# Optimization experiments

Measured on AMD Instinct MI355X. Metric: run time of the kernel, lower is better.

The kernel has to match this reference:

```python
import jax, jax.numpy as jnp
import numpy as np

N_SL, H, W, D = 64, 128, 128, 128
D_MODEL, D_INNER, N_LAYERS, N_HEAD = 256, 512, 4, 4
RES_RATIO = 1.0
N_ITER_CG = 2

def _gauss_psf(shape=(3, 3, 3), sigma=1.0):
    ax = [np.arange(s) - (s - 1) / 2.0 for s in shape]
    gz, gy, gx = np.meshgrid(*ax, indexing='ij')
    k = np.exp(-(gx ** 2 + gy ** 2 + gz ** 2) / (2 * sigma ** 2))
    return jnp.asarray((k / k.sum()).astype(np.float32))

def _rigid_transforms():
    rng = np.random.default_rng(0)
    a = rng.uniform(-0.3, 0.3, (N_SL, 3)).astype(np.float32)
    t = rng.uniform(-8.0, 8.0, (N_SL, 3)).astype(np.float32)
    z = np.zeros(N_SL, np.float32); o = np.ones(N_SL, np.float32)
    cz, sz = np.cos(a[:, 2]), np.sin(a[:, 2])
    cy, sy = np.cos(a[:, 1]), np.sin(a[:, 1])
    cx, sx = np.cos(a[:, 0]), np.sin(a[:, 0])
    Rz = np.stack([cz, -sz, z, sz, cz, z, z, z, o], -1).reshape(-1, 3, 3)
    Ry = np.stack([cy, z, sy, z, o, z, -sy, z, cy], -1).reshape(-1, 3, 3)
    Rx = np.stack([o, z, z, z, cx, -sx, z, sx, cx], -1).reshape(-1, 3, 3)
    R = Rz @ Ry @ Rx
    return jnp.asarray(np.concatenate([R, t[:, :, None]], -1).astype(np.float32))

def _slice_points():
    xs = (jnp.arange(W, dtype=jnp.float32) - (W - 1) / 2.0) * RES_RATIO
    ys = (jnp.arange(H, dtype=jnp.float32) - (H - 1) / 2.0) * RES_RATIO
    gy, gx = jnp.meshgrid(ys, xs, indexing='ij')
    return jnp.stack([gx.ravel(), gy.ravel(), jnp.zeros(H * W, jnp.float32)], -1)

def _psf_grid(psf):
    kz, ky, kx = psf.shape
    oz = jnp.arange(kz, dtype=jnp.float32) - (kz - 1) / 2.0
    oy = jnp.arange(ky, dtype=jnp.float32) - (ky - 1) / 2.0
    ox = jnp.arange(kx, dtype=jnp.float32) - (kx - 1) / 2.0
    gz, gy, gx = jnp.meshgrid(oz, oy, ox, indexing='ij')
    return jnp.stack([gx.ravel(), gy.ravel(), gz.ravel()], -1), psf.ravel()

def _tri_gather(vol, c):
    Dz, Dy, Dx = vol.shape
    x, y, z = c[..., 0], c[..., 1], c[..., 2]
    x0, y0, z0 = jnp.floor(x), jnp.floor(y), jnp.floor(z)
    fx, fy, fz = x - x0, y - y0, z - z0
    out = jnp.zeros(x.shape, vol.dtype)
    for dz in (0, 1):
        for dy in (0, 1):
            for dx in (0, 1):
                xi, yi, zi = x0 + dx, y0 + dy, z0 + dz
                w = (fx if dx else 1 - fx) * (fy if dy else 1 - fy) * (fz if dz else 1 - fz)
                ok = (xi >= 0) & (xi < Dx) & (yi >= 0) & (yi < Dy) & (zi >= 0) & (zi < Dz)
                xi = jnp.clip(xi, 0, Dx - 1).astype(jnp.int32)
                yi = jnp.clip(yi, 0, Dy - 1).astype(jnp.int32)
                zi = jnp.clip(zi, 0, Dz - 1).astype(jnp.int32)
                out = out + jnp.where(ok, w * vol[zi, yi, xi], 0.0)
    return out

def _tri_scatter(vflat, c, vals, shape):
    Dz, Dy, Dx = shape
    x, y, z = c[..., 0], c[..., 1], c[..., 2]
    x0, y0, z0 = jnp.floor(x), jnp.floor(y), jnp.floor(z)
    fx, fy, fz = x - x0, y - y0, z - z0
    for dz in (0, 1):
        for dy in (0, 1):
            for dx in (0, 1):
                xi, yi, zi = x0 + dx, y0 + dy, z0 + dz
                w = (fx if dx else 1 - fx) * (fy if dy else 1 - fy) * (fz if dz else 1 - fz)
                ok = (xi >= 0) & (xi < Dx) & (yi >= 0) & (yi < Dy) & (zi >= 0) & (zi < Dz)
                xi = jnp.clip(xi, 0, Dx - 1).astype(jnp.int32)
                yi = jnp.clip(yi, 0, Dy - 1).astype(jnp.int32)
                zi = jnp.clip(zi, 0, Dz - 1).astype(jnp.int32)
                idx = (zi * Dy + yi) * Dx + xi
                vflat = vflat.at[idx.ravel()].add(jnp.where(ok, w * vals, 0.0).ravel())
    return vflat

def _slice_acq(transforms, volume, slices_mask, psf):
    vol = volume[0, 0]
    R, t = transforms[:, :, :3], transforms[:, :, 3]
    pts = _slice_points()
    offs, pw = _psf_grid(psf)
    ctr = jnp.array([(vol.shape[2] - 1) / 2.0, (vol.shape[1] - 1) / 2.0, (vol.shape[0] - 1) / 2.0], jnp.float32)
    def body(acc, ow):
        o, w = ow
        world = jnp.einsum('nij,pj->npi', R, pts + o) + t[:, None, :]
        return acc + w * _tri_gather(vol, world + ctr), None
    acc, _ = jax.lax.scan(jax.checkpoint(body), jnp.zeros((transforms.shape[0], H * W), jnp.float32), (offs, pw))
    out = acc.reshape(-1, 1, H, W)
    if slices_mask is not None:
        out = out * slices_mask
    return out

def _slice_acq_adj(transforms, psf, slices, slices_mask, vol_shape):
    vals = slices.reshape(slices.shape[0], -1)
    if slices_mask is not None:
        vals = vals * slices_mask.reshape(slices.shape[0], -1)
    R, t = transforms[:, :, :3], transforms[:, :, 3]
    pts = _slice_points()
    offs, pw = _psf_grid(psf)
    Dz, Dy, Dx = vol_shape
    ctr = jnp.array([(Dx - 1) / 2.0, (Dy - 1) / 2.0, (Dz - 1) / 2.0], jnp.float32)
    def body(vf, ow):
        o, w = ow
        world = jnp.einsum('nij,pj->npi', R, pts + o) + t[:, None, :] + ctr
        return _tri_scatter(vf, world, w * vals, vol_shape), None
    vf, _ = jax.lax.scan(jax.checkpoint(body), jnp.zeros(Dz * Dy * Dx, jnp.float32), (offs, pw))
    return vf.reshape(1, 1, Dz, Dy, Dx)

def _gaussian_blur(x, sigma=1.0, ks=3):
    ax = np.arange(ks) - (ks - 1) / 2.0
    k1 = np.exp(-ax ** 2 / (2 * sigma ** 2))
    k2 = np.outer(k1, k1); k2 = k2 / k2.sum()
    w = jnp.asarray(k2.astype(np.float32)).reshape(1, 1, ks, ks)
    return jax.lax.conv_general_dilated(x, w, (1, 1), 'SAME', dimension_numbers=('NCHW', 'OIHW', 'NCHW'))

def _conv(x, w, stride=1):
    return jax.lax.conv_general_dilated(x, w, (stride, stride), 'SAME', dimension_numbers=('NCHW', 'OIHW', 'NCHW'))

def _cg(AtA, b, x, n_iter):
    r = b - AtA(x)
    p = r
    rr = jnp.vdot(r, r)
    for _ in range(n_iter):
        Ap = AtA(p)
        alpha = rr / jnp.vdot(p, Ap)
        x = x + alpha * p
        r = r - alpha * Ap
        rr2 = jnp.vdot(r, r)
        p = r + (rr2 / rr) * p
        rr = rr2
    return x

def _ln(x, g, b):
    m = x.mean(-1, keepdims=True)
    v = ((x - m) ** 2).mean(-1, keepdims=True)
    return (x - m) / jnp.sqrt(v + 1e-5) * g + b

def _mha(h, wq, wk, wv, wo):
    n, dm = h.shape
    dk = dm // N_HEAD
    q = (h @ wq).reshape(n, N_HEAD, dk)
    k = (h @ wk).reshape(n, N_HEAD, dk)
    v = (h @ wv).reshape(n, N_HEAD, dk)
    att = jax.nn.softmax(jnp.einsum('qhd,khd->hqk', q, k) / jnp.sqrt(jnp.float32(dk)), -1)
    return jnp.einsum('hqk,khd->qhd', att, v).reshape(n, dm) @ wo

def _forward(theta, transforms, slices, volume, psf, idx, conv1_w, b1_w1, b1_w2, b2_w1, b2_w2, b2_proj, b3_w1, b3_w2, b3_proj, pos_w, pos_b, wq, wk, wv, wo, ln1_g, ln1_b, ff1_w, ff1_b, ff2_w, ff2_b, ln2_g, ln2_b, fc_w, fc_b):
    mask = (_gaussian_blur(slices) > 0).astype(slices.dtype)
    slices_est = _slice_acq(transforms, volume, mask, psf)
    z = jnp.concatenate([slices, slices_est], 1)
    hc = jax.nn.relu(_conv(z, conv1_w, 2))
    r = _conv(jax.nn.relu(_conv(hc, b1_w1)), b1_w2)
    hc = jax.nn.relu(hc + r)
    r = _conv(jax.nn.relu(_conv(hc, b2_w1, 2)), b2_w2)
    hc = jax.nn.relu(_conv(hc, b2_proj, 2) + r)
    r = _conv(jax.nn.relu(_conv(hc, b3_w1, 2)), b3_w2)
    hc = jax.nn.relu(_conv(hc, b3_proj, 2) + r)
    feat = hc.mean((2, 3))
    pe = jnp.concatenate([theta, idx], -1) @ pos_w + pos_b
    hs = feat + pe
    for l in range(N_LAYERS):
        hs = _ln(hs + _mha(hs, wq[l], wk[l], wv[l], wo[l]), ln1_g[l], ln1_b[l])
        ff = jax.nn.relu(hs @ ff1_w[l] + ff1_b[l]) @ ff2_w[l] + ff2_b[l]
        hs = _ln(hs + ff, ln2_g[l], ln2_b[l])
    x = hs @ fc_w + fc_b
    x = jax.nn.softmax(x, axis=0) * x.shape[0]
    x = jnp.minimum(x, 3.0)
    p = x.reshape(-1, 1, 1, 1)
    vol_shape = volume.shape[2:]
    At = lambda s: _slice_acq_adj(transforms, psf, s, mask, vol_shape)
    AtA = lambda v: At(_slice_acq(transforms, v, mask, psf) * p)
    b = At(slices * p)
    vol = _cg(AtA, b, volume, N_ITER_CG)
    return jax.nn.relu(vol), x

def setup_inputs():
    key = jax.random.key(0)
    ks = jax.random.split(key, 24)
    def nrm(k, shp, s=0.05):
        return jax.random.normal(k, shp, jnp.float32) * s
    yy, xx = jnp.meshgrid(jnp.arange(H, dtype=jnp.float32), jnp.arange(W, dtype=jnp.float32), indexing='ij')
    disk = (((yy - (H - 1) / 2) ** 2 + (xx - (W - 1) / 2) ** 2) < (0.45 * W) ** 2).astype(jnp.float32)
    slices = jax.random.uniform(ks[0], (N_SL, 1, H, W), jnp.float32) * disk
    return {
        'theta': nrm(ks[1], (N_SL, 6), 0.1),
        'transforms': _rigid_transforms(),
        'slices': slices,
        'volume': jax.random.uniform(ks[2], (1, 1, D, H, W), jnp.float32) * 0.1,
        'psf': _gauss_psf(),
        'idx': jnp.tile(jnp.arange(N_SL, dtype=jnp.float32).reshape(-1, 1) / N_SL, (1, 2)),
        'conv1_w': nrm(ks[3], (64, 2, 7, 7)),
        'b1_w1': nrm(ks[4], (64, 64, 3, 3)),
        'b1_w2': nrm(ks[5], (64, 64, 3, 3)),
        'b2_w1': nrm(ks[6], (128, 64, 3, 3)),
        'b2_w2': nrm(ks[7], (128, 128, 3, 3)),
        'b2_proj': nrm(ks[8], (128, 64, 1, 1)),
        'b3_w1': nrm(ks[9], (256, 128, 3, 3)),
        'b3_w2': nrm(ks[10], (256, 256, 3, 3)),
        'b3_proj': nrm(ks[11], (256, 128, 1, 1)),
        'pos_w': nrm(ks[12], (8, D_MODEL)),
        'pos_b': jnp.zeros((D_MODEL,), jnp.float32),
        'wq': nrm(ks[13], (N_LAYERS, D_MODEL, D_MODEL)),
        'wk': nrm(ks[14], (N_LAYERS, D_MODEL, D_MODEL)),
        'wv': nrm(ks[15], (N_LAYERS, D_MODEL, D_MODEL)),
        'wo': nrm(ks[16], (N_LAYERS, D_MODEL, D_MODEL)),
        'ln1_g': jnp.ones((N_LAYERS, D_MODEL), jnp.float32),
        'ln1_b': jnp.zeros((N_LAYERS, D_MODEL), jnp.float32),
        'ff1_w': nrm(ks[17], (N_LAYERS, D_MODEL, D_INNER)),
        'ff1_b': jnp.zeros((N_LAYERS, D_INNER), jnp.float32),
        'ff2_w': nrm(ks[18], (N_LAYERS, D_INNER, D_MODEL)),
        'ff2_b': jnp.zeros((N_LAYERS, D_MODEL), jnp.float32),
        'ln2_g': jnp.ones((N_LAYERS, D_MODEL), jnp.float32),
        'ln2_b': jnp.zeros((N_LAYERS, D_MODEL), jnp.float32),
        'fc_w': nrm(ks[19], (D_MODEL, 1)),
        'fc_b': jnp.zeros((1,), jnp.float32),
    }

def reference(theta, transforms, slices, volume, psf, idx, conv1_w, b1_w1, b1_w2, b2_w1, b2_w2, b2_proj, b3_w1, b3_w2, b3_proj, pos_w, pos_b, wq, wk, wv, wo, ln1_g, ln1_b, ff1_w, ff1_b, ff2_w, ff2_b, ln2_g, ln2_b, fc_w, fc_b):
    return _forward(theta, transforms, slices, volume, psf, idx, conv1_w, b1_w1, b1_w2, b2_w1, b2_w2, b2_proj, b3_w1, b3_w2, b3_proj, pos_w, pos_b, wq, wk, wv, wo, ln1_g, ln1_b, ff1_w, ff1_b, ff2_w, ff2_b, ln2_g, ln2_b, fc_w, fc_b)
```

## Files before the change

### kernel.cpp

```cpp
#include <hip/hip_runtime.h>
#include <hip/hip_bf16.h>

#define NSL 64
#define NPX 16384
#define VN  2097152
#define PCL 16900
#define PCS 50700
#define PCN 3244800

__global__ void k_prep(const float* __restrict__ tr, const float* __restrict__ psf,
                       float* __restrict__ Rm, float* __restrict__ pw)
{
  int n = threadIdx.x;
  if (n < 27) pw[n] = psf[n];
  if (n >= NSL) return;
  #pragma unroll
  for (int i = 0; i < 3; i++){
    #pragma unroll
    for (int j = 0; j < 3; j++) Rm[n*12 + i*3 + j] = tr[n*12 + i*4 + j];
    Rm[n*12 + 9 + i] = tr[n*12 + i*4 + 3];
  }
}

__global__ void k_mask(const float* __restrict__ slices, float* __restrict__ mask)
{
  int gid = blockIdx.x*256 + threadIdx.x;
  if (gid >= NSL*NPX) return;
  int n = gid >> 14, p = gid & 16383;
  int py = p >> 7, px = p & 127;
  const float* s = slices + n*NPX;
  bool any = false;
  for (int dy = -1; dy <= 1; dy++){
    int yy = py + dy;
    if ((unsigned)yy >= 128u) continue;
    for (int dx = -1; dx <= 1; dx++){
      int xx = px + dx;
      if ((unsigned)xx >= 128u) continue;
      any = any || (s[yy*128 + xx] > 0.f);
    }
  }
  mask[gid] = any ? 1.f : 0.f;
}

__global__ void k_volcopy(const float* __restrict__ v, float* __restrict__ o)
{
  int gid = blockIdx.x*256 + threadIdx.x;
  if (gid < VN) o[gid] = v[gid];
}

__global__ void k_copy0(const float* __restrict__ slices, float* __restrict__ z)
{
  int gid = blockIdx.x*256 + threadIdx.x;
  if (gid >= NSL*NPX) return;
  int n = gid >> 14, p = gid & 16383;
  z[n*2*NPX + p] = slices[gid];
}

__global__ void k_premul(const float* __restrict__ s, const float* __restrict__ mask,
                         const float* __restrict__ ps, float* __restrict__ o)
{
  int gid = blockIdx.x*256 + threadIdx.x;
  if (gid >= NSL*NPX) return;
  float v = s[gid] * mask[gid];
  if (ps) v *= ps[gid >> 14];
  o[gid] = v;
}

__device__ __forceinline__ float lerpf(float a, float b, float t){ return fmaf(t, b-a, a); }

__device__ __forceinline__ float tri_gather(const float* __restrict__ vol, float x, float y, float z)
{
  float xf = floorf(x), yf = floorf(y), zf = floorf(z);
  int x0 = (int)xf, y0 = (int)yf, z0 = (int)zf;
  float fx = x - xf, fy = y - yf, fz = z - zf;
  if ((unsigned)x0 < 127u && (unsigned)y0 < 127u && (unsigned)z0 < 127u){
    const float* p = vol + (z0*128 + y0)*128 + x0;
    float c00 = lerpf(p[0],     p[1],     fx);
    float c01 = lerpf(p[128],   p[129],   fx);
    float c10 = lerpf(p[16384], p[16385], fx);
    float c11 = lerpf(p[16512], p[16513], fx);
    return lerpf(lerpf(c00, c01, fy), lerpf(c10, c11, fy), fz);
  }
  float gx0 = 1.f - fx, gy0 = 1.f - fy, gz0 = 1.f - fz;
  bool vx0 = (unsigned)x0 < 128u, vx1 = (unsigned)(x0+1) < 128u;
  bool vy0 = (unsigned)y0 < 128u, vy1 = (unsigned)(y0+1) < 128u;
  bool vz0 = (unsigned)z0 < 128u, vz1 = (unsigned)(z0+1) < 128u;
  int i0 = (z0*128 + y0)*128 + x0;
  float acc = 0.f;
  if (vz0){
    if (vy0){
      if (vx0) acc += gx0*gy0*gz0 * vol[i0];
      if (vx1) acc += fx *gy0*gz0 * vol[i0+1];
    }
    if (vy1){
      if (vx0) acc += gx0*fy*gz0 * vol[i0+128];
      if (vx1) acc += fx *fy*gz0 * vol[i0+129];
    }
  }
  if (vz1){
    int i1 = i0 + 16384;
    if (vy0){
      if (vx0) acc += gx0*gy0*fz * vol[i1];
      if (vx1) acc += fx *gy0*fz * vol[i1+1];
    }
    if (vy1){
      if (vx0) acc += gx0*fy*fz * vol[i1+128];
      if (vx1) acc += fx *fy*fz * vol[i1+129];
    }
  }
  return acc;
}

__global__ void k_gather(const float* __restrict__ vol, const float* __restrict__ Rm,
                         const float* __restrict__ pw, const float* __restrict__ mask,
                         const float* __restrict__ ps, float* __restrict__ out,
                         int outStride, int outOff)
{
  int gid = blockIdx.x*256 + threadIdx.x;
  int n = gid >> 14;
  __shared__ float srm[12];
  __shared__ float sdof[27][3];
  __shared__ float spw[27];
  if (threadIdx.x < 12) srm[threadIdx.x] = Rm[n*12 + threadIdx.x];
  __syncthreads();
  if (threadIdx.x < 27){
    int k = threadIdx.x;
    float ox = (float)(k % 3) - 1.f;
    float oy = (float)((k/3) % 3) - 1.f;
    float oz = (float)(k/9) - 1.f;
    sdof[k][0] = srm[0]*ox + srm[1]*oy + srm[2]*oz;
    sdof[k][1] = srm[3]*ox + srm[4]*oy + srm[5]*oz;
    sdof[k][2] = srm[6]*ox + srm[7]*oy + srm[8]*oz;
    spw[k] = pw[k];
  }
  __syncthreads();
  int p = gid & 16383;
  int py = p >> 7, px = p & 127;
  float gx = (float)px - 63.5f, gy = (float)py - 63.5f;
  float bx = srm[0]*gx + srm[1]*gy + srm[9]  + 63.5f;
  float by = srm[3]*gx + srm[4]*gy + srm[10] + 63.5f;
  float bz = srm[6]*gx + srm[7]*gy + srm[11] + 63.5f;
  float acc = 0.f;
  for (int k = 0; k < 27; k += 3){
    float g0 = tri_gather(vol, bx+sdof[k  ][0], by+sdof[k  ][1], bz+sdof[k  ][2]);
    float g1 = tri_gather(vol, bx+sdof[k+1][0], by+sdof[k+1][1], bz+sdof[k+1][2]);
    float g2 = tri_gather(vol, bx+sdof[k+2][0], by+sdof[k+2][1], bz+sdof[k+2][2]);
    acc += spw[k]*g0 + spw[k+1]*g1 + spw[k+2]*g2;
  }
  float v = acc * mask[gid];
  if (ps) v *= ps[n];
  out[n*outStride + outOff + p] = v;
}

__global__ void k_pcorr(const float* __restrict__ val, const float* __restrict__ pw,
                        float* __restrict__ out)
{
  int gid = blockIdx.x*256 + threadIdx.x;
  if (gid >= PCN) return;
  int n = gid / PCS;
  int r = gid % PCS;
  int l = r / PCL;
  int q = r % PCL;
  int my = q / 130 - 1, mx = q % 130 - 1;
  const float* vs = val + n*NPX;
  const float* pg = pw + l*9;
  float inner = 0.f;
  #pragma unroll
  for (int oy = -1; oy <= 1; oy++){
    int qy = my - oy;
    if ((unsigned)qy >= 128u) continue;
    const float* vrow = vs + qy*128;
    const float* pr = pg + (oy+1)*3;
    #pragma unroll
    for (int ox = -1; ox <= 1; ox++){
      int qx = mx - ox;
      if ((unsigned)qx >= 128u) continue;
      inner += pr[ox+1] * vrow[qx];
    }
  }
  out[gid] = inner;
}

__global__ __launch_bounds__(256, 4) void k_sadj(
    const float* __restrict__ pcor,
    const float* __restrict__ Rm,
    float* __restrict__ out)
{
  __shared__ float sR[NSL*12];
  __shared__ int   slist[NSL];
  __shared__ int   scnt;
  int tid = threadIdx.x;
  for (int i = tid; i < NSL*12; i += 256) sR[i] = Rm[i];
  __syncthreads();

  int b  = blockIdx.x;
  int bx = (b & 15) * 8;
  int by = ((b >> 4) & 15) * 8;
  int bz = (b >> 8) * 4;

  if (tid < 64){
    const float* R = &sR[tid*12];
    float axc = ((float)bx + 3.5f) - 63.5f - R[9];
    float ayc = ((float)by + 3.5f) - 63.5f - R[10];
    float azc = ((float)bz + 1.5f) - 63.5f - R[11];
    float Zc = R[2]*axc + R[5]*ayc + R[8]*azc;
    float rZ = fabsf(R[2])*3.5f + fabsf(R[5])*3.5f + fabsf(R[8])*1.5f;
    bool ok = fabsf(Zc) < 2.7321f + rZ;
    if (ok){
      float Pc = R[0]*axc + R[3]*ayc + R[6]*azc + 63.5f;
      float rP = fabsf(R[0])*3.5f + fabsf(R[3])*3.5f + fabsf(R[6])*1.5f;
      float Qc = R[1]*axc + R[4]*ayc + R[7]*azc + 63.5f;
      float rQ = fabsf(R[1])*3.5f + fabsf(R[4])*3.5f + fabsf(R[7])*1.5f;
      ok = (Pc + rP > -2.7321f) && (Pc - rP < 130.7321f)
        && (Qc + rQ > -2.7321f) && (Qc - rQ < 130.7321f);
    }
    unsigned long long m = __ballot(ok);
    if (ok) slist[__popcll(m & ((1ull << tid) - 1ull))] = tid;
    if (tid == 0) scnt = (int)__popcll(m);
  }
  __syncthreads();
  int cnt = scnt;

  int lx = tid & 7, ly = (tid >> 3) & 7, lz = tid >> 6;
  int vx = bx + lx, vy = by + ly, vz = bz + lz;

  float cvx = (float)vx - 63.5f;
  float cvy = (float)vy - 63.5f;
  float cvz = (float)vz - 63.5f;

  float acc = 0.f;
  for (int i = 0; i < cnt; i++){
    int n = slist[i];
    const float* R = &sR[n*12];
    float ax = cvx - R[9], ay = cvy - R[10], az = cvz - R[11];
    float Z = R[2]*ax + R[5]*ay + R[8]*az;
    if (fabsf(Z) >= 2.7321f) continue;
    float P = R[0]*ax + R[3]*ay + R[6]*az + 63.5f;
    float Q = R[1]*ax + R[4]*ay + R[7]*az + 63.5f;
    if (P <= -2.7321f || P >= 130.7321f || Q <= -2.7321f || Q >= 130.7321f) continue;
    const float* pc = pcor + n*PCS;

    #pragma unroll
    for (int mz = -1; mz <= 1; mz++){
      float dz = (float)mz - Z;
      float rem2 = 3.f - dz*dz;
      if (rem2 <= 0.f) continue;
      float sy = sqrtf(rem2);
      int my0 = (int)ceilf(Q - sy), my1 = (int)floorf(Q + sy);
      if (my0 < -1) my0 = -1;
      if (my1 > 128) my1 = 128;
      const float* pl = pc + (mz+1)*PCL;
      for (int my = my0; my <= my1; my++){
        float dy = (float)my - Q;
        float rem1 = rem2 - dy*dy;
        if (rem1 <= 0.f) continue;
        float sx = sqrtf(rem1);
        int mx0 = (int)ceilf(P - sx), mx1 = (int)floorf(P + sx);
        if (mx0 < -1) mx0 = -1;
        if (mx1 > 128) mx1 = 128;
        float dx = (float)mx0 - P;
        float rx = R[0]*dx + R[1]*dy + R[2]*dz;
        float ry = R[3]*dx + R[4]*dy + R[5]*dz;
        float rz = R[6]*dx + R[7]*dy + R[8]*dz;
        const float* crow = pl + (my+1)*130 + (mx0+1);
        for (int mx = mx0; mx <= mx1; mx++){
          float w3 = fmaxf(1.f - fabsf(rx), 0.f)
                   * fmaxf(1.f - fabsf(ry), 0.f)
                   * fmaxf(1.f - fabsf(rz), 0.f);
          if (w3 > 0.f) acc += w3 * crow[mx - mx0];
          rx += R[0]; ry += R[3]; rz += R[6];
        }
      }
    }
  }
  out[(vz*128 + vy)*128 + vx] = acc;
}

template<int K, int S, int TILE, int CC, int COT>
__global__ __launch_bounds__(256, 2) void k_convt(
    const float* __restrict__ in, const float* __restrict__ wt,
    const float* __restrict__ res, float* __restrict__ out,
    int Cin, int Hin, int Cout, int Hout,
    int pad, int relu, int nBG, int spTiles)
{
  constexpr int BPB  = 1024 / (TILE*TILE);
  constexpr int ITX  = (K==1) ? TILE : (TILE-1)*S + K;
  constexpr int ITP  = ITX | 1;
  constexpr int KK   = K*K;
  constexpr int PERB = TILE*TILE/4;
  constexpr int RS   = (K==1) ? 1 : S;
  constexpr int NIN  = (CC*ITX*ITX + PERB - 1)/PERB;
  constexpr int NWT  = (COT*CC*KK + 255)/256;

  __shared__ float sIn[BPB*CC*ITX*ITP];
  __shared__ float sW[CC*KK*COT];

  int tid = threadIdx.x;
  int bl  = tid / PERB;
  int t2  = tid % PERB;
  int tx  = t2 % TILE;
  int tyq = (t2 / TILE) * 4;

  int bid = blockIdx.x;
  int spT = bid % spTiles; bid /= spTiles;
  int bG  = bid % nBG;     bid /= nBG;
  int coT = bid;
  int b0  = bG * BPB;

  int tpr = Hout / TILE;
  int ox0 = (spT % tpr) * TILE;
  int oy0 = (spT / tpr) * TILE;
  int co0 = coT * COT;
  int ix0 = ox0*S - pad;
  int iy0 = oy0*S - pad;

  float acc[COT*4];
  #pragma unroll
  for (int i = 0; i < COT*4; i++) acc[i] = 0.f;

  for (int ci0 = 0; ci0 < Cin; ci0 += CC){
    #pragma unroll
    for (int it = 0; it < NWT; it++){
      int i = tid + it*256;
      if (i < COT*CC*KK){
        int co = i / (CC*KK);
        int r  = i % (CC*KK);
        sW[r*COT + co] = wt[((size_t)(co0+co)*Cin + ci0 + r/KK)*KK + (r % KK)];
      }
    }
    #pragma unroll
    for (int it = 0; it < NIN; it++){
      int i = t2 + it*PERB;
      if (i < CC*ITX*ITX){
        int cc = i / (ITX*ITX);
        int r  = i % (ITX*ITX);
        int yy = r / ITX, xx = r % ITX;
        int gy = (K==1) ? iy0 + yy*S : iy0 + yy;
        int gx = (K==1) ? ix0 + xx*S : ix0 + xx;
        float v = 0.f;
        if ((unsigned)gy < (unsigned)Hin && (unsigned)gx < (unsigned)Hin)
          v = in[(((size_t)(b0+bl)*Cin + ci0+cc)*Hin + gy)*Hin + gx];
        sIn[((bl*CC + cc)*ITX + yy)*ITP + xx] = v;
      }
    }
    __syncthreads();

    #pragma unroll
    for (int cc = 0; cc < CC; cc++){
      const float* ip = &sIn[(bl*CC + cc)*ITX*ITP];
      #pragma unroll
      for (int ky = 0; ky < K; ky++){
        #pragma unroll
        for (int kx = 0; kx < K; kx++){
          int xi = (K==1) ? tx : tx*S + kx;
          int yb = (K==1) ? tyq : tyq*S + ky;
          float v0 = ip[(yb       )*ITP + xi];
          float v1 = ip[(yb +   RS)*ITP + xi];
          float v2 = ip[(yb + 2*RS)*ITP + xi];
          float v3 = ip[(yb + 3*RS)*ITP + xi];
          const float4* wv = (const float4*)&sW[(cc*KK + ky*K + kx)*COT];
          #pragma unroll
          for (int g = 0; g < COT/4; g++){
            float4 w = wv[g];
            acc[(g*4+0)*4+0] += w.x*v0; acc[(g*4+0)*4+1] += w.x*v1;
            acc[(g*4+0)*4+2] += w.x*v2; acc[(g*4+0)*4+3] += w.x*v3;
            acc[(g*4+1)*4+0] += w.y*v0; acc[(g*4+1)*4+1] += w.y*v1;
            acc[(g*4+1)*4+2] += w.y*v2; acc[(g*4+1)*4+3] += w.y*v3;
            acc[(g*4+2)*4+0] += w.z*v0; acc[(g*4+2)*4+1] += w.z*v1;
            acc[(g*4+2)*4+2] += w.z*v2; acc[(g*4+2)*4+3] += w.z*v3;
            acc[(g*4+3)*4+0] += w.w*v0; acc[(g*4+3)*4+1] += w.w*v1;
            acc[(g*4+3)*4+2] += w.w*v2; acc[(g*4+3)*4+3] += w.w*v3;
          }
        }
      }
    }
    __syncthreads();
  }

  int b = b0 + bl;
  #pragma unroll
  for (int co = 0; co < COT; co++){
    size_t base = (((size_t)b*Cout + co0+co)*Hout + oy0 + tyq)*Hout + ox0 + tx;
    #pragma unroll
    for (int r = 0; r < 4; r++){
      float v = acc[co*4 + r];
      if (res) v += res[base + (size_t)r*Hout];
      if (relu) v = fmaxf(v, 0.f);
      out[base + (size_t)r*Hout] = v;
    }
  }
}

template<int K, int S, int TILE, int COT, int CCW>
__global__ __launch_bounds__(256, 2) void k_convd(
    const float* __restrict__ in, const float* __restrict__ wt,
    const float* __restrict__ res, float* __restrict__ out,
    int Cin, int Hin, int Cout, int Hout,
    int pad, int relu, int nBG, int spTiles, int swz)
{
  constexpr int PERB = TILE*TILE/4;
  constexpr int BPB  = 1024 / (TILE*TILE);
  constexpr int KK   = K*K;
  constexpr int NW   = (CCW*KK*COT + 255)/256;

  __shared__ float sW[CCW*KK*COT];

  int tid = threadIdx.x;
  int bl  = tid / PERB;
  int t2  = tid % PERB;
  int tx  = t2 % TILE;
  int tyq = (t2 / TILE) * 4;

  int bid = blockIdx.x;
  int spT, bG, coT;
  if (swz){
    int nCo = Cout / COT;
    int u = bid & 7; bid >>= 3;
    coT = bid % nCo; bid /= nCo;
    int tile = bid * 8 + u;
    spT = tile % spTiles;
    bG  = tile / spTiles;
  } else {
    spT = bid % spTiles; bid /= spTiles;
    bG  = bid % nBG;     bid /= nBG;
    coT = bid;
  }
  int b0  = bG * BPB;

  int tpr = Hout / TILE;
  int ox0 = (spT % tpr) * TILE;
  int oy0 = (spT / tpr) * TILE;
  int co0 = coT * COT;

  int b  = b0 + bl;
  int ix = (ox0 + tx)*S - pad;
  int iy = (oy0 + tyq)*S - pad;

  bool okx[K];
  #pragma unroll
  for (int kx = 0; kx < K; kx++) okx[kx] = (unsigned)(ix + kx) < (unsigned)Hin;
  bool oky[4*K];
  #pragma unroll
  for (int r = 0; r < 4; r++){
    #pragma unroll
    for (int ky = 0; ky < K; ky++)
      oky[r*K + ky] = (unsigned)(iy + r*S + ky) < (unsigned)Hin;
  }

  float acc[COT*4];
  #pragma unroll
  for (int i = 0; i < COT*4; i++) acc[i] = 0.f;

  size_t chs = (size_t)Hin*Hin;
  const float* ipb = in + (size_t)b*Cin*chs + (iy*Hin + ix);

  for (int ci0 = 0; ci0 < Cin; ci0 += CCW){
    if (ci0) __syncthreads();
    #pragma unroll
    for (int it = 0; it < NW; it++){
      int i = tid + it*256;
      if (i < CCW*KK*COT){
        int co = i % COT;
        int r  = i / COT;
        sW[i] = wt[((size_t)(co0+co)*Cin + ci0 + r/KK)*KK + (r % KK)];
      }
    }
    __syncthreads();

    const float* ip = ipb + (size_t)ci0*chs;
    for (int cc = 0; cc < CCW; cc++, ip += chs){
      #pragma unroll
      for (int ky = 0; ky < K; ky++){
        #pragma unroll
        for (int kx = 0; kx < K; kx++){
          const float* rp = ip + ky*Hin + kx;
          float t0 = rp[0];
          float t1 = rp[S*Hin];
          float t2 = rp[2*S*Hin];
          float t3 = rp[3*S*Hin];
          float v0 = (oky[0*K+ky] && okx[kx]) ? t0 : 0.f;
          float v1 = (oky[1*K+ky] && okx[kx]) ? t1 : 0.f;
          float v2 = (oky[2*K+ky] && okx[kx]) ? t2 : 0.f;
          float v3 = (oky[3*K+ky] && okx[kx]) ? t3 : 0.f;
          const float4* wv = (const float4*)&sW[(cc*KK + ky*K + kx)*COT];
          #pragma unroll
          for (int g = 0; g < COT/4; g++){
            float4 w = wv[g];
            acc[(g*4+0)*4+0] += w.x*v0; acc[(g*4+0)*4+1] += w.x*v1;
            acc[(g*4+0)*4+2] += w.x*v2; acc[(g*4+0)*4+3] += w.x*v3;
            acc[(g*4+1)*4+0] += w.y*v0; acc[(g*4+1)*4+1] += w.y*v1;
            acc[(g*4+1)*4+2] += w.y*v2; acc[(g*4+1)*4+3] += w.y*v3;
            acc[(g*4+2)*4+0] += w.z*v0; acc[(g*4+2)*4+1] += w.z*v1;
            acc[(g*4+2)*4+2] += w.z*v2; acc[(g*4+2)*4+3] += w.z*v3;
            acc[(g*4+3)*4+0] += w.w*v0; acc[(g*4+3)*4+1] += w.w*v1;
            acc[(g*4+3)*4+2] += w.w*v2; acc[(g*4+3)*4+3] += w.w*v3;
          }
        }
      }
    }
  }

  #pragma unroll
  for (int co = 0; co < COT; co++){
    size_t base = (((size_t)b*Cout + co0+co)*Hout + oy0 + tyq)*Hout + ox0 + tx;
    #pragma unroll
    for (int r = 0; r < 4; r++){
      float v = acc[co*4 + r];
      if (res) v += res[base + (size_t)r*Hout];
      if (relu) v = fmaxf(v, 0.f);
      out[base + (size_t)r*Hout] = v;
    }
  }
}

__global__ void k_pool(const float* __restrict__ in, float* __restrict__ feat, int cnt)
{
  int gid = blockIdx.x*256 + threadIdx.x;
  if (gid >= cnt) return;
  const float* p = in + (size_t)gid*256;
  float s = 0.f;
  for (int i = 0; i < 256; i++) s += p[i];
  feat[gid] = s * (1.f/256.f);
}

__global__ void k_pe(const float* __restrict__ feat, const float* __restrict__ theta,
                     const float* __restrict__ idxin, const float* __restrict__ pos_w,
                     const float* __restrict__ pos_b, float* __restrict__ hs)
{
  int gid = blockIdx.x*256 + threadIdx.x;
  if (gid >= 64*256) return;
  int n = gid >> 8, d = gid & 255;
  float s = pos_b[d];
  #pragma unroll
  for (int j = 0; j < 6; j++) s += theta[n*6+j] * pos_w[j*256+d];
  #pragma unroll
  for (int j = 0; j < 2; j++) s += idxin[n*2+j] * pos_w[(6+j)*256+d];
  hs[gid] = feat[gid] + s;
}

__global__ void k_qkv(const float* __restrict__ hs, const float* __restrict__ wq,
                      const float* __restrict__ wk, const float* __restrict__ wv,
                      float* __restrict__ qkv)
{
  int gid = blockIdx.x*256 + threadIdx.x;
  if (gid >= 64*768) return;
  int n = gid / 768, m = gid % 768;
  int which = m >> 8, j = m & 255;
  const float* w = (which == 0) ? wq : (which == 1) ? wk : wv;
  const float* h = hs + n*256;
  float s = 0.f;
  for (int i = 0; i < 256; i++) s += h[i] * w[i*256 + j];
  qkv[which*16384 + n*256 + j] = s;
}

__global__ void k_attn(const float* __restrict__ qkv, float* __restrict__ aout)
{
  int h = blockIdx.x;
  int tid = threadIdx.x;
  __shared__ float sc[4096];
  const float* q  = qkv + h*64;
  const float* kk = qkv + 16384 + h*64;
  const float* v  = qkv + 32768 + h*64;
  for (int idx = tid; idx < 4096; idx += 256){
    int qi = idx >> 6, ki = idx & 63;
    float s = 0.f;
    for (int d = 0; d < 64; d++) s += q[qi*256+d] * kk[ki*256+d];
    sc[idx] = s * 0.125f;
  }
  __syncthreads();
  if (tid < 64){
    float mx = -1e30f;
    for (int k = 0; k < 64; k++) mx = fmaxf(mx, sc[tid*64+k]);
    float sum = 0.f;
    for (int k = 0; k < 64; k++){ float e = __expf(sc[tid*64+k]-mx); sc[tid*64+k] = e; sum += e; }
    float inv = 1.f/sum;
    for (int k = 0; k < 64; k++) sc[tid*64+k] *= inv;
  }
  __syncthreads();
  for (int idx = tid; idx < 4096; idx += 256){
    int qi = idx >> 6, d = idx & 63;
    float s = 0.f;
    for (int ki = 0; ki < 64; ki++) s += sc[qi*64+ki] * v[ki*256+d];
    aout[qi*256 + h*64 + d] = s;
  }
}

__global__ void k_proj_ln(const float* __restrict__ ain, const float* __restrict__ wo,
                          const float* __restrict__ g, const float* __restrict__ bb,
                          float* __restrict__ hs)
{
  int n = blockIdx.x, d = threadIdx.x;
  __shared__ float row[256];
  __shared__ float red[256];
  __shared__ float smean, svar;
  row[d] = ain[n*256+d];
  __syncthreads();
  float s = hs[n*256+d];
  for (int i = 0; i < 256; i++) s += row[i] * wo[i*256+d];
  red[d] = s; __syncthreads();
  for (int off = 128; off; off >>= 1){ if (d < off) red[d] += red[d+off]; __syncthreads(); }
  if (d == 0) smean = red[0] * (1.f/256.f);
  __syncthreads();
  float c = s - smean;
  red[d] = c*c; __syncthreads();
  for (int off = 128; off; off >>= 1){ if (d < off) red[d] += red[d+off]; __syncthreads(); }
  if (d == 0) svar = red[0] * (1.f/256.f);
  __syncthreads();
  hs[n*256+d] = c * rsqrtf(svar + 1e-5f) * g[d] + bb[d];
}

__global__ void k_ff1(const float* __restrict__ hs, const float* __restrict__ w,
                      const float* __restrict__ b, float* __restrict__ h1)
{
  int gid = blockIdx.x*256 + threadIdx.x;
  if (gid >= 64*512) return;
  int n = gid >> 9, j = gid & 511;
  float s = b[j];
  const float* h = hs + n*256;
  for (int i = 0; i < 256; i++) s += h[i] * w[i*512 + j];
  h1[gid] = fmaxf(s, 0.f);
}

__global__ void k_ff2_ln(const float* __restrict__ h1, const float* __restrict__ w,
                         const float* __restrict__ b, const float* __restrict__ g,
                         const float* __restrict__ bb, float* __restrict__ hs)
{
  int n = blockIdx.x, d = threadIdx.x;
  __shared__ float row[512];
  __shared__ float red[256];
  __shared__ float smean, svar;
  row[d] = h1[n*512+d];
  row[d+256] = h1[n*512+256+d];
  __syncthreads();
  float s = hs[n*256+d] + b[d];
  for (int i = 0; i < 512; i++) s += row[i] * w[i*256+d];
  red[d] = s; __syncthreads();
  for (int off = 128; off; off >>= 1){ if (d < off) red[d] += red[d+off]; __syncthreads(); }
  if (d == 0) smean = red[0] * (1.f/256.f);
  __syncthreads();
  float c = s - smean;
  red[d] = c*c; __syncthreads();
  for (int off = 128; off; off >>= 1){ if (d < off) red[d] += red[d+off]; __syncthreads(); }
  if (d == 0) svar = red[0] * (1.f/256.f);
  __syncthreads();
  hs[n*256+d] = c * rsqrtf(svar + 1e-5f) * g[d] + bb[d];
}

__global__ void k_head(const float* __restrict__ hs, const float* __restrict__ fcw,
                       const float* __restrict__ fcb, float* __restrict__ pvec,
                       float* __restrict__ outx)
{
  int n = threadIdx.x;
  float s = fcb[0];
  const float* h = hs + n*256;
  for (int i = 0; i < 256; i++) s += h[i] * fcw[i];
  __shared__ float xs[64];
  xs[n] = s;
  __syncthreads();
  float mx = -1e30f;
  for (int i = 0; i < 64; i++) mx = fmaxf(mx, xs[i]);
  float sum = 0.f;
  for (int i = 0; i < 64; i++) sum += __expf(xs[i]-mx);
  float val = __expf(s-mx)/sum * 64.f;
  val = fminf(val, 3.f);
  pvec[n] = val;
  outx[n] = val;
}

__global__ void k_dot(const float* __restrict__ a, const float* __restrict__ b,
                      float* __restrict__ scal, int slot, int n)
{
  int gid = blockIdx.x*blockDim.x + threadIdx.x;
  int stride = gridDim.x*blockDim.x;
  float s = 0.f;
  for (int i = gid; i < n; i += stride) s += a[i]*b[i];
  for (int off = 32; off; off >>= 1) s += __shfl_down(s, off, 64);
  __shared__ float wsum[4];
  int lane = threadIdx.x & 63, wv = threadIdx.x >> 6;
  if (lane == 0) wsum[wv] = s;
  __syncthreads();
  if (threadIdx.x == 0) atomicAdd(&scal[slot], wsum[0]+wsum[1]+wsum[2]+wsum[3]);
}

__global__ void k_rinit(const float* __restrict__ b, const float* __restrict__ A,
                        float* __restrict__ r, float* __restrict__ p)
{
  int gid = blockIdx.x*256 + threadIdx.x;
  if (gid < VN){ float v = b[gid] - A[gid]; r[gid] = v; p[gid] = v; }
}

__global__ void k_xr(float* __restrict__ x, const float* __restrict__ p,
                     float* __restrict__ r, const float* __restrict__ Ap,
                     const float* __restrict__ scal, int sa, int sb)
{
  int gid = blockIdx.x*256 + threadIdx.x;
  if (gid < VN){
    float a = scal[sa] / scal[sb];
    x[gid] += a * p[gid];
    r[gid] -= a * Ap[gid];
  }
}

__global__ void k_pupd(float* __restrict__ p, const float* __restrict__ r,
                       const float* __restrict__ scal, int sa, int sb)
{
  int gid = blockIdx.x*256 + threadIdx.x;
  if (gid < VN){ float b = scal[sa] / scal[sb]; p[gid] = r[gid] + b * p[gid]; }
}

__global__ void k_xfin(const float* __restrict__ x, const float* __restrict__ p,
                       const float* __restrict__ scal, int sa, int sb,
                       float* __restrict__ out)
{
  int gid = blockIdx.x*256 + threadIdx.x;
  if (gid < VN) out[gid] = fmaxf(x[gid] + (scal[sa] / scal[sb]) * p[gid], 0.f);
}

extern "C" void kernel_launch(void* const* d_in, const int* in_sizes, int n_in,
                              void* d_out, int out_size, void* d_ws, size_t ws_size,
                              hipStream_t stream)
{
  const float* theta      = (const float*)d_in[0];
  const float* transforms = (const float*)d_in[1];
  const float* slices     = (const float*)d_in[2];
  const float* volume     = (const float*)d_in[3];
  const float* psf        = (const float*)d_in[4];
  const float* idxv       = (const float*)d_in[5];

  char* wsp = (char*)d_ws;
  auto carve = [&](size_t bytes)->void*{
    void* r = (void*)wsp; wsp += (bytes + 255) & ~(size_t)255; return r;
  };
  float* scal = (float*)carve(16*4);
  float* Rm   = (float*)carve(768*4);
  float* pw   = (float*)carve(32*4);
  float* pvec = (float*)carve(64*4);
  float* feat = (float*)carve(16384*4);
  float* hs   = (float*)carve(16384*4);
  float* qkv  = (float*)carve(49152*4);
  float* aout = (float*)carve(16384*4);
  float* h1   = (float*)carve(32768*4);
  float* mask = (float*)carve((size_t)NSL*NPX*4);
  float* volA = (float*)carve((size_t)VN*4);

  size_t used  = (size_t)(wsp - (char*)d_ws);
  size_t avail = (ws_size > used) ? ws_size - used : 0;
  size_t cgU   = ((size_t)4*VN + 2*(size_t)NSL*NPX + (size_t)PCN)*4;
  auto needU = [&](int cb)->size_t{
    size_t u = ((size_t)VN + 3*(size_t)cb*262144)*4;
    return (u > cgU) ? u : cgU;
  };
  int CB = 8;
  if (avail >= needU(64) + 4096) CB = 64;
  else if (avail >= needU(32) + 4096) CB = 32;

  size_t cbe = (size_t)CB*262144;
  float* U    = (float*)carve(needU(CB));
  float* z    = U;
  float* bufA = U + VN;
  float* bufB = bufA + cbe;
  float* bufC = bufB + cbe;
  float* bvol = U;
  float* rvol = U + VN;
  float* pvol = U + 2*(size_t)VN;
  float* Avol = U + 3*(size_t)VN;
  float* sscr = U + 4*(size_t)VN;
  float* bval = sscr + (size_t)NSL*NPX;
  float* pcor = bval + (size_t)NSL*NPX;

  hipMemsetAsync(scal, 0, 64, stream);
  k_prep<<<1, 64, 0, stream>>>(transforms, psf, Rm, pw);
  k_mask<<<4096, 256, 0, stream>>>(slices, mask);
  k_volcopy<<<8192, 256, 0, stream>>>(volume, volA);
  k_gather<<<4096, 256, 0, stream>>>(volA, Rm, pw, mask, nullptr, z, 2*NPX, NPX);
  k_copy0<<<4096, 256, 0, stream>>>(slices, z);

  const float* w6  = (const float*)d_in[6];
  const float* w7  = (const float*)d_in[7];
  const float* w8  = (const float*)d_in[8];
  const float* w9  = (const float*)d_in[9];
  const float* w10 = (const float*)d_in[10];
  const float* w11 = (const float*)d_in[11];
  const float* w12 = (const float*)d_in[12];
  const float* w13 = (const float*)d_in[13];
  const float* w14 = (const float*)d_in[14];

  for (int c = 0; c < 64/CB; c++){
    const float* zc = z + (size_t)c*CB*2*NPX;
    k_convt<7,2,32,2,16><<<CB*16, 256, 0, stream>>>(zc,  w6,  nullptr, bufA, 2,  128, 64,  64, 2, 1, CB, 4);
    k_convd<3,1,32,16,16><<<CB*16, 256, 0, stream>>>(bufA, w7,  nullptr, bufB, 64, 64,  64,  64, 1, 1, CB, 4, 1);
    k_convd<3,1,32,16,16><<<CB*16, 256, 0, stream>>>(bufB, w8,  bufA,    bufC, 64, 64,  64,  64, 1, 1, CB, 4, 1);
    k_convd<3,2,32,16,16><<<CB*8,  256, 0, stream>>>(bufC, w9,  nullptr, bufA, 64, 64,  128, 32, 0, 1, CB, 1, 0);
    k_convd<1,2,32,16,64><<<CB*8,  256, 0, stream>>>(bufC, w11, nullptr, bufB, 64, 64,  128, 32, 0, 0, CB, 1, 0);
    k_convd<3,1,32,16,16><<<CB*8,  256, 0, stream>>>(bufA, w10, bufB,    bufC, 128,32,  128, 32, 1, 1, CB, 1, 0);
    k_convd<3,2,16,8,32><<<(CB/4)*32, 256, 0, stream>>>(bufC, w12, nullptr, bufA, 128, 32, 256, 16, 0, 1, CB/4, 1, 0);
    k_convd<1,2,16,8,128><<<(CB/4)*32, 256, 0, stream>>>(bufC, w14, nullptr, bufB, 128, 32, 256, 16, 0, 0, CB/4, 1, 0);
    k_convd<3,1,16,8,32><<<(CB/4)*32, 256, 0, stream>>>(bufA, w13, bufB,    bufC, 256, 16, 256, 16, 1, 1, CB/4, 1, 0);
    k_pool<<<CB, 256, 0, stream>>>(bufC, feat + (size_t)c*CB*256, CB*256);
  }

  k_pe<<<64, 256, 0, stream>>>(feat, theta, idxv, (const float*)d_in[15], (const float*)d_in[16], hs);
  for (int l = 0; l < 4; l++){
    k_qkv<<<192, 256, 0, stream>>>(hs, (const float*)d_in[17] + (size_t)l*65536,
                                       (const float*)d_in[18] + (size_t)l*65536,
                                       (const float*)d_in[19] + (size_t)l*65536, qkv);
    k_attn<<<4, 256, 0, stream>>>(qkv, aout);
    k_proj_ln<<<64, 256, 0, stream>>>(aout, (const float*)d_in[20] + (size_t)l*65536,
                                      (const float*)d_in[21] + l*256, (const float*)d_in[22] + l*256, hs);
    k_ff1<<<128, 256, 0, stream>>>(hs, (const float*)d_in[23] + (size_t)l*131072,
                                   (const float*)d_in[24] + l*512, h1);
    k_ff2_ln<<<64, 256, 0, stream>>>(h1, (const float*)d_in[25] + (size_t)l*131072,
                                     (const float*)d_in[26] + l*256, (const float*)d_in[27] + l*256,
                                     (const float*)d_in[28] + l*256, hs);
  }
  k_head<<<1, 64, 0, stream>>>(hs, (const float*)d_in[29], (const float*)d_in[30], pvec,
                               (float*)d_out + VN);

  const int PCB = (PCN + 255)/256;
  k_premul<<<4096, 256, 0, stream>>>(slices, mask, pvec, bval);
  k_pcorr<<<PCB, 256, 0, stream>>>(bval, pw, pcor);
  k_sadj<<<8192, 256, 0, stream>>>(pcor, Rm, bvol);
  k_gather<<<4096, 256, 0, stream>>>(volA, Rm, pw, mask, pvec, sscr, NPX, 0);
  k_pcorr<<<PCB, 256, 0, stream>>>(sscr, pw, pcor);
  k_sadj<<<8192, 256, 0, stream>>>(pcor, Rm, Avol);
  k_rinit<<<8192, 256, 0, stream>>>(bvol, Avol, rvol, pvol);
  k_dot<<<512, 256, 0, stream>>>(rvol, rvol, scal, 0, VN);
  k_gather<<<4096, 256, 0, stream>>>(pvol, Rm, pw, mask, pvec, sscr, NPX, 0);
  k_pcorr<<<PCB, 256, 0, stream>>>(sscr, pw, pcor);
  k_sadj<<<8192, 256, 0, stream>>>(pcor, Rm, Avol);
  k_dot<<<512, 256, 0, stream>>>(pvol, Avol, scal, 1, VN);
  k_xr<<<8192, 256, 0, stream>>>(volA, pvol, rvol, Avol, scal, 0, 1);
  k_dot<<<512, 256, 0, stream>>>(rvol, rvol, scal, 3, VN);
  k_pupd<<<8192, 256, 0, stream>>>(pvol, rvol, scal, 3, 0);
  k_gather<<<4096, 256, 0, stream>>>(pvol, Rm, pw, mask, pvec, sscr, NPX, 0);
  k_pcorr<<<PCB, 256, 0, stream>>>(sscr, pw, pcor);
  k_sadj<<<8192, 256, 0, stream>>>(pcor, Rm, Avol);
  k_dot<<<512, 256, 0, stream>>>(pvol, Avol, scal, 5, VN);
  k_xfin<<<8192, 256, 0, stream>>>(volA, pvol, scal, 3, 5, (float*)d_out);
}
```

Baseline: 4.667 ms.

## Split PSF gather into grid-point trilinear sampling plus separate 27-tap correlation

Since the slice transform is rigid, the PSF offsets map to a fixed 3x130x130 lattice in slice coordinates. Each trilinear sample is now computed once per lattice point into a buffer, and a second kernel applies the 27-tap PSF weights from that buffer. This replaces 27 trilinear gathers per pixel with about 3 samples per pixel plus cheap stencil reads. The cost is an extra buffer write and read and one more kernel launch. Separately, the forward projection of the unchanged initial volume is reused from the stored z buffer by scaling it instead of being recomputed.

```diff
diff --git a/kernel.cpp b/kernel.cpp
--- a/kernel.cpp
+++ b/kernel.cpp
@@ -66,6 +66,15 @@
   o[gid] = v;
 }
 
+__global__ void k_zscale(const float* __restrict__ z, const float* __restrict__ ps,
+                         float* __restrict__ out)
+{
+  int gid = blockIdx.x*256 + threadIdx.x;
+  if (gid >= NSL*NPX) return;
+  int n = gid >> 14, p = gid & 16383;
+  out[gid] = z[n*2*NPX + NPX + p] * ps[n];
+}
+
 __device__ __forceinline__ float lerpf(float a, float b, float t){ return fmaf(t, b-a, a); }
 
 __device__ __forceinline__ float tri_gather(const float* __restrict__ vol, float x, float y, float z)
@@ -111,45 +120,45 @@
   return acc;
 }
 
-__global__ void k_gather(const float* __restrict__ vol, const float* __restrict__ Rm,
-                         const float* __restrict__ pw, const float* __restrict__ mask,
-                         const float* __restrict__ ps, float* __restrict__ out,
-                         int outStride, int outOff)
-{
+__global__ void k_gvol(const float* __restrict__ vol, const float* __restrict__ Rm,
+                       float* __restrict__ out)
+{
+  int gid = blockIdx.x*256 + threadIdx.x;
+  if (gid >= PCN) return;
+  int n = gid / PCS;
+  int r = gid % PCS;
+  int w = r / PCL - 1;
+  int q = r % PCL;
+  int v = q / 130 - 1, u = q % 130 - 1;
+  const float* R = Rm + n*12;
+  float fu = (float)u - 63.5f, fv = (float)v - 63.5f, fw = (float)w;
+  float x = R[0]*fu + R[1]*fv + R[2]*fw + R[9]  + 63.5f;
+  float y = R[3]*fu + R[4]*fv + R[5]*fw + R[10] + 63.5f;
+  float z = R[6]*fu + R[7]*fv + R[8]*fw + R[11] + 63.5f;
+  out[gid] = tri_gather(vol, x, y, z);
+}
+
+__global__ void k_gcorr(const float* __restrict__ G, const float* __restrict__ pw,
+                        const float* __restrict__ mask, const float* __restrict__ ps,
+                        float* __restrict__ out, int outStride, int outOff)
+{
+  __shared__ float spw[27];
+  if (threadIdx.x < 27) spw[threadIdx.x] = pw[threadIdx.x];
+  __syncthreads();
   int gid = blockIdx.x*256 + threadIdx.x;
   int n = gid >> 14;
-  __shared__ float srm[12];
-  __shared__ float sdof[27][3];
-  __shared__ float spw[27];
-  if (threadIdx.x < 12) srm[threadIdx.x] = Rm[n*12 + threadIdx.x];
-  __syncthreads();
-  if (threadIdx.x < 27){
-    int k = threadIdx.x;
-    float ox = (float)(k % 3) - 1.f;
-    float oy = (float)((k/3) % 3) - 1.f;
-    float oz = (float)(k/9) - 1.f;
-    sdof[k][0] = srm[0]*ox + srm[1]*oy + srm[2]*oz;
-    sdof[k][1] = srm[3]*ox + srm[4]*oy + srm[5]*oz;
-    sdof[k][2] = srm[6]*ox + srm[7]*oy + srm[8]*oz;
-    spw[k] = pw[k];
-  }
-  __syncthreads();
   int p = gid & 16383;
   int py = p >> 7, px = p & 127;
-  float gx = (float)px - 63.5f, gy = (float)py - 63.5f;
-  float bx = srm[0]*gx + srm[1]*gy + srm[9]  + 63.5f;
-  float by = srm[3]*gx + srm[4]*gy + srm[10] + 63.5f;
-  float bz = srm[6]*gx + srm[7]*gy + srm[11] + 63.5f;
+  const float* Gn = G + n*PCS;
   float acc = 0.f;
-  for (int k = 0; k < 27; k += 3){
-    float g0 = tri_gather(vol, bx+sdof[k  ][0], by+sdof[k  ][1], bz+sdof[k  ][2]);
-    float g1 = tri_gather(vol, bx+sdof[k+1][0], by+sdof[k+1][1], bz+sdof[k+1][2]);
-    float g2 = tri_gather(vol, bx+sdof[k+2][0], by+sdof[k+2][1], bz+sdof[k+2][2]);
-    acc += spw[k]*g0 + spw[k+1]*g1 + spw[k+2]*g2;
-  }
-  float v = acc * mask[gid];
-  if (ps) v *= ps[n];
-  out[n*outStride + outOff + p] = v;
+  #pragma unroll
+  for (int k = 0; k < 27; k++){
+    int ox = k % 3, oy = (k/3) % 3, oz = k/9;
+    acc += spw[k] * Gn[oz*PCL + (py+oy)*130 + (px+ox)];
+  }
+  float val = acc * mask[gid];
+  if (ps) val *= ps[n];
+  out[n*outStride + outOff + p] = val;
 }
 
 __global__ void k_pcorr(const float* __restrict__ val, const float* __restrict__ pw,
@@ -768,11 +777,14 @@
   float* bval = sscr + (size_t)NSL*NPX;
   float* pcor = bval + (size_t)NSL*NPX;
 
+  const int PCB = PCN/256;
+
   hipMemsetAsync(scal, 0, 64, stream);
   k_prep<<<1, 64, 0, stream>>>(transforms, psf, Rm, pw);
   k_mask<<<4096, 256, 0, stream>>>(slices, mask);
   k_volcopy<<<8192, 256, 0, stream>>>(volume, volA);
-  k_gather<<<4096, 256, 0, stream>>>(volA, Rm, pw, mask, nullptr, z, 2*NPX, NPX);
+  k_gvol<<<PCB, 256, 0, stream>>>(volA, Rm, pcor);
+  k_gcorr<<<4096, 256, 0, stream>>>(pcor, pw, mask, nullptr, z, 2*NPX, NPX);
   k_copy0<<<4096, 256, 0, stream>>>(slices, z);
 
   const float* w6  = (const float*)d_in[6];
@@ -816,23 +828,24 @@
   k_head<<<1, 64, 0, stream>>>(hs, (const float*)d_in[29], (const float*)d_in[30], pvec,
                                (float*)d_out + VN);
 
-  const int PCB = (PCN + 255)/256;
+  k_zscale<<<4096, 256, 0, stream>>>(z, pvec, sscr);
   k_premul<<<4096, 256, 0, stream>>>(slices, mask, pvec, bval);
   k_pcorr<<<PCB, 256, 0, stream>>>(bval, pw, pcor);
   k_sadj<<<8192, 256, 0, stream>>>(pcor, Rm, bvol);
-  k_gather<<<4096, 256, 0, stream>>>(volA, Rm, pw, mask, pvec, sscr, NPX, 0);
   k_pcorr<<<PCB, 256, 0, stream>>>(sscr, pw, pcor);
   k_sadj<<<8192, 256, 0, stream>>>(pcor, Rm, Avol);
   k_rinit<<<8192, 256, 0, stream>>>(bvol, Avol, rvol, pvol);
   k_dot<<<512, 256, 0, stream>>>(rvol, rvol, scal, 0, VN);
-  k_gather<<<4096, 256, 0, stream>>>(pvol, Rm, pw, mask, pvec, sscr, NPX, 0);
+  k_gvol<<<PCB, 256, 0, stream>>>(pvol, Rm, pcor);
+  k_gcorr<<<4096, 256, 0, stream>>>(pcor, pw, mask, pvec, sscr, NPX, 0);
   k_pcorr<<<PCB, 256, 0, stream>>>(sscr, pw, pcor);
   k_sadj<<<8192, 256, 0, stream>>>(pcor, Rm, Avol);
   k_dot<<<512, 256, 0, stream>>>(pvol, Avol, scal, 1, VN);
   k_xr<<<8192, 256, 0, stream>>>(volA, pvol, rvol, Avol, scal, 0, 1);
   k_dot<<<512, 256, 0, stream>>>(rvol, rvol, scal, 3, VN);
   k_pupd<<<8192, 256, 0, stream>>>(pvol, rvol, scal, 3, 0);
-  k_gather<<<4096, 256, 0, stream>>>(pvol, Rm, pw, mask, pvec, sscr, NPX, 0);
+  k_gvol<<<PCB, 256, 0, stream>>>(pvol, Rm, pcor);
+  k_gcorr<<<4096, 256, 0, stream>>>(pcor, pw, mask, pvec, sscr, NPX, 0);
   k_pcorr<<<PCB, 256, 0, stream>>>(sscr, pw, pcor);
   k_sadj<<<8192, 256, 0, stream>>>(pcor, Rm, Avol);
   k_dot<<<512, 256, 0, stream>>>(pvol, Avol, scal, 5, VN);
```

Result: faster. 4.457 ms (median of 2 runs) (-4.5%).
